# Optimization experiments

Hardware: AMD Instinct MI355X
Metric: run time of the kernel (lower is better)

## Reference

```python
import jax, jax.numpy as jnp
import numpy as np

F = 2048          # frame length = len(window_function) = n_fft
HOP = F // 2      # step_length (overlap=2, perfect reconstruction)
B = 8             # signals / channels
T = 1 << 20       # samples per signal (multiple of HOP)


def setup_inputs() -> dict:
    key = jax.random.key(0)
    x = jax.random.normal(key, (B, T), dtype=jnp.float32)
    # cosine (sine) window, the standard MDCT deringing window
    n = jnp.arange(F, dtype=jnp.float32)
    window = jnp.sin(jnp.pi * (n + 0.5) / F).astype(jnp.float32)
    return {"x": x, "window": window}


def reference(x, window):
    # Batched, fused version of the serial per-frame twiddle-FFT-twiddle MDCT.
    F_ = window.shape[0]
    hop = F_ // 2
    N = F_ // 2                      # output bins per frame (odd-stacked)
    # center=True: pad F/2 zeros on both sides so first/last frames are centered
    xp = jnp.pad(x, ((0, 0), (hop, hop)))
    n_frames = (xp.shape[1] - F_) // hop + 1
    starts = jnp.arange(n_frames) * hop                       # [nf]
    frames = xp[:, starts[:, None] + jnp.arange(F_)]          # [B, nf, F]
    # pre-twiddle: exp(-i*pi*n/(2N)), n = 0..2N-1
    pre = jnp.exp(-1j * jnp.pi * jnp.arange(F_) / F_).astype(jnp.complex64)
    # post-twiddle: exp(-i*pi*n0*(k+0.5)/N), n0 = (N+1)/2
    n0 = (N + 1) / 2.0
    post = jnp.exp(-1j * jnp.pi * n0 * (jnp.arange(N) + 0.5) / N).astype(jnp.complex64)
    # window + pre-twiddle, one batched FFT over all frames, truncate to N bins
    Xc = jnp.fft.fft((frames * window).astype(jnp.complex64) * pre, axis=-1)[..., :N]
    # real part * post-twiddle phase, scale sqrt(1/N)*sqrt(2)
    out = jnp.real(Xc * post) * np.float32(np.sqrt(2.0 / N))
    return out.astype(jnp.float32)          # [B, n_frames, N]
```

## Files before the change

### kernel.cpp

```cpp
#include <hip/hip_runtime.h>
#include <cmath>

#define BATCH   8
#define TLEN    1048576
#define NFRM    1025
#define MROWS   (BATCH * NFRM)

#define SWZ(i) ((i) ^ (((i) >> 4) & 15))

__global__ __launch_bounds__(128)
void mdct_fft_kernel(const float* __restrict__ x,
                     const float* __restrict__ w,
                     float* __restrict__ out)
{
    __shared__ float2 zz[2][512];
    float2* const za = zz[0];
    float2* const zb = zz[1];
    float*  const uf = (float*)zz[1];

    const int r   = blockIdx.x;
    const int tid = threadIdx.x;
    const int b = r / NFRM;
    const int t = r - b * NFRM;

    {
        const float* xb = x + b * TLEN + (t - 1) * 1024;
        {
            const int p  = tid * 4;
            float4 res = {0.0f, 0.0f, 0.0f, 0.0f};
            if (t != NFRM - 1) {
                const int rb = 1532 - p;
                const int fb = 1536 + p;
                float4 xr = *(const float4*)(xb + rb);
                float4 wr = *(const float4*)(w  + rb);
                float4 xf = *(const float4*)(xb + fb);
                float4 wf = *(const float4*)(w  + fb);
                res.x = -(wr.w * xr.w + wf.x * xf.x);
                res.y = -(wr.z * xr.z + wf.y * xf.y);
                res.z = -(wr.y * xr.y + wf.z * xf.z);
                res.w = -(wr.x * xr.x + wf.w * xf.w);
            }
            *(float4*)&uf[p] = res;
        }
        {
            const int p  = 512 + tid * 4;
            float4 res = {0.0f, 0.0f, 0.0f, 0.0f};
            if (t != 0) {
                const int rb = 1532 - p;
                const int fb = p - 512;
                float4 xr = *(const float4*)(xb + rb);
                float4 wr = *(const float4*)(w  + rb);
                float4 xf = *(const float4*)(xb + fb);
                float4 wf = *(const float4*)(w  + fb);
                res.x = wf.x * xf.x - wr.w * xr.w;
                res.y = wf.y * xf.y - wr.z * xr.z;
                res.z = wf.z * xf.z - wr.y * xr.y;
                res.w = wf.w * xf.w - wr.x * xr.x;
            }
            *(float4*)&uf[p] = res;
        }
    }
    __syncthreads();

#pragma unroll
    for (int h = 0; h < 4; ++h) {
        int n = tid + h * 128;
        float re = uf[2 * n];
        float im = uf[1023 - 2 * n];
        float a = (float)(4 * n + 1) * (1.0f / 4096.0f);
        float c = cospif(a), s = sinpif(a);
        za[SWZ(n)] = make_float2(re * c + im * s, im * c - re * s);
    }
    __syncthreads();

    float2* X = za;
    float2* Y = zb;
#pragma unroll
    for (int j = 0; j < 4; ++j) {
        const int ls = 2 * j;
        const int s  = 1 << ls;
        const int mh = 256 >> ls;
        const int p = tid >> ls;
        float2 P0 = X[SWZ(tid)];
        float2 P1 = X[SWZ(tid + 128)];
        float2 P2 = X[SWZ(tid + 256)];
        float2 P3 = X[SWZ(tid + 384)];
        float ang = (float)p * (1.0f / (float)mh);
        float c1 = cospif(ang), s1 = sinpif(ang);
        float c2 = c1 * c1 - s1 * s1, s2 = 2.0f * c1 * s1;
        float c3 = c1 * c2 - s1 * s2, s3 = s1 * c2 + c1 * s2;
        float sax = P0.x + P2.x, say = P0.y + P2.y;
        float sbx = P1.x + P3.x, sby = P1.y + P3.y;
        float dax = P0.x - P2.x, day = P0.y - P2.y;
        float dbx = P1.x - P3.x, dby = P1.y - P3.y;
        const int o = tid + 3 * s * p;
        Y[SWZ(o)] = make_float2(sax + sbx, say + sby);
        float e1x = dax + dby, e1y = day - dbx;
        Y[SWZ(o + s)] = make_float2(e1x * c1 + e1y * s1, e1y * c1 - e1x * s1);
        float e2x = sax - sbx, e2y = say - sby;
        Y[SWZ(o + 2 * s)] = make_float2(e2x * c2 + e2y * s2, e2y * c2 - e2x * s2);
        float e3x = dax - dby, e3y = day + dbx;
        Y[SWZ(o + 3 * s)] = make_float2(e3x * c3 + e3y * s3, e3y * c3 - e3x * s3);
        float2* tmp = X; X = Y; Y = tmp;
        __syncthreads();
    }

#pragma unroll
    for (int hh = 0; hh < 2; ++hh) {
        int k0 = tid + hh * 128;
        float2 A  = X[SWZ(k0)];
        float2 Bv = X[SWZ(k0 + 256)];
        float zr[2] = {A.x + Bv.x, A.x - Bv.x};
        float zi[2] = {A.y + Bv.y, A.y - Bv.y};
#pragma unroll
        for (int h = 0; h < 2; ++h) {
            int k = k0 + h * 256;
            float a = (float)(4 * k + 1) * (1.0f / 4096.0f);
            float c = cospif(a), s = sinpif(a);
            float re = zr[h] * c + zi[h] * s;
            float im = zi[h] * c - zr[h] * s;
            uf[2 * k]        =  re * 0.04419417382415922f;
            uf[1023 - 2 * k] = -im * 0.04419417382415922f;
        }
    }
    __syncthreads();

    *(float4*)&out[r * 1024 + tid * 4]       = *(const float4*)&uf[tid * 4];
    *(float4*)&out[r * 1024 + 512 + tid * 4] = *(const float4*)&uf[512 + tid * 4];
}

extern "C" void kernel_launch(void* const* d_in, const int* in_sizes, int n_in,
                              void* d_out, int out_size, void* d_ws, size_t ws_size,
                              hipStream_t stream) {
    const float* x = (const float*)d_in[0];
    const float* w = (const float*)d_in[1];
    float* out = (float*)d_out;
    (void)d_ws; (void)ws_size;

    mdct_fft_kernel<<<MROWS, 128, 0, stream>>>(x, w, out);
}
```

Before: 93.18 us.

## Assign one frame per wavefront and fuse pre-twiddle into first radix-4 stage

Each 128-thread block now processes two frames, one per 64-lane wavefront, with each wave keeping its own shared-memory buffers. This lets every block-wide __syncthreads be replaced by a wave-level barrier, and the first radix-4 FFT stage is folded into the pre-twiddle pass, saving one shared-memory round trip. Each lane now handles twice as many points, which raises per-thread work and register pressure and doubles LDS use per block.

```diff
diff --git a/kernel.cpp b/kernel.cpp
--- a/kernel.cpp
+++ b/kernel.cpp
@@ -13,20 +13,24 @@
                      const float* __restrict__ w,
                      float* __restrict__ out)
 {
-    __shared__ float2 zz[2][512];
-    float2* const za = zz[0];
-    float2* const zb = zz[1];
-    float*  const uf = (float*)zz[1];
+    __shared__ float2 zz[2][2][512];
+    const int wid  = threadIdx.x >> 6;
+    const int lane = threadIdx.x & 63;
+    float2* const za = zz[wid][0];
+    float2* const zb = zz[wid][1];
+    float*  const uf = (float*)zz[wid][1];
 
-    const int r   = blockIdx.x;
-    const int tid = threadIdx.x;
+    const int r = blockIdx.x * 2 + wid;
     const int b = r / NFRM;
     const int t = r - b * NFRM;
 
-    {
-        const float* xb = x + b * TLEN + (t - 1) * 1024;
+    const float* xb = x + b * TLEN + (t - 1) * 1024;
+
+#pragma unroll
+    for (int sl = 0; sl < 2; ++sl) {
+        const int tt = lane + sl * 64;
         {
-            const int p  = tid * 4;
+            const int p  = tt * 4;
             float4 res = {0.0f, 0.0f, 0.0f, 0.0f};
             if (t != NFRM - 1) {
                 const int rb = 1532 - p;
@@ -43,7 +47,7 @@
             *(float4*)&uf[p] = res;
         }
         {
-            const int p  = 512 + tid * 4;
+            const int p  = 512 + tt * 4;
             float4 res = {0.0f, 0.0f, 0.0f, 0.0f};
             if (t != 0) {
                 const int rb = 1532 - p;
@@ -60,73 +64,119 @@
             *(float4*)&uf[p] = res;
         }
     }
-    __syncthreads();
+    __builtin_amdgcn_wave_barrier();
 
 #pragma unroll
-    for (int h = 0; h < 4; ++h) {
-        int n = tid + h * 128;
-        float re = uf[2 * n];
-        float im = uf[1023 - 2 * n];
-        float a = (float)(4 * n + 1) * (1.0f / 4096.0f);
-        float c = cospif(a), s = sinpif(a);
-        za[SWZ(n)] = make_float2(re * c + im * s, im * c - re * s);
+    for (int sl = 0; sl < 2; ++sl) {
+        const int tt = lane + sl * 64;
+        float px[4], py[4];
+#pragma unroll
+        for (int h = 0; h < 4; ++h) {
+            const int n = tt + h * 128;
+            float re = uf[2 * n];
+            float im = uf[1023 - 2 * n];
+            float a = (float)(4 * n + 1) * (1.0f / 4096.0f);
+            float c = cospif(a), s = sinpif(a);
+            px[h] = re * c + im * s;
+            py[h] = im * c - re * s;
+        }
+        float ang = (float)tt * (1.0f / 256.0f);
+        float c1 = cospif(ang), s1 = sinpif(ang);
+        float c2 = c1 * c1 - s1 * s1, s2 = 2.0f * c1 * s1;
+        float c3 = c1 * c2 - s1 * s2, s3 = s1 * c2 + c1 * s2;
+        float sax = px[0] + px[2], say = py[0] + py[2];
+        float sbx = px[1] + px[3], sby = py[1] + py[3];
+        float dax = px[0] - px[2], day = py[0] - py[2];
+        float dbx = px[1] - px[3], dby = py[1] - py[3];
+        const int o = 4 * tt;
+        za[SWZ(o)] = make_float2(sax + sbx, say + sby);
+        float e1x = dax + dby, e1y = day - dbx;
+        za[SWZ(o + 1)] = make_float2(e1x * c1 + e1y * s1, e1y * c1 - e1x * s1);
+        float e2x = sax - sbx, e2y = say - sby;
+        za[SWZ(o + 2)] = make_float2(e2x * c2 + e2y * s2, e2y * c2 - e2x * s2);
+        float e3x = dax - dby, e3y = day + dbx;
+        za[SWZ(o + 3)] = make_float2(e3x * c3 + e3y * s3, e3y * c3 - e3x * s3);
     }
-    __syncthreads();
+    __builtin_amdgcn_wave_barrier();
 
     float2* X = za;
     float2* Y = zb;
 #pragma unroll
-    for (int j = 0; j < 4; ++j) {
+    for (int j = 1; j < 4; ++j) {
         const int ls = 2 * j;
         const int s  = 1 << ls;
         const int mh = 256 >> ls;
-        const int p = tid >> ls;
-        float2 P0 = X[SWZ(tid)];
-        float2 P1 = X[SWZ(tid + 128)];
-        float2 P2 = X[SWZ(tid + 256)];
-        float2 P3 = X[SWZ(tid + 384)];
-        float ang = (float)p * (1.0f / (float)mh);
-        float c1 = cospif(ang), s1 = sinpif(ang);
-        float c2 = c1 * c1 - s1 * s1, s2 = 2.0f * c1 * s1;
-        float c3 = c1 * c2 - s1 * s2, s3 = s1 * c2 + c1 * s2;
-        float sax = P0.x + P2.x, say = P0.y + P2.y;
-        float sbx = P1.x + P3.x, sby = P1.y + P3.y;
-        float dax = P0.x - P2.x, day = P0.y - P2.y;
-        float dbx = P1.x - P3.x, dby = P1.y - P3.y;
-        const int o = tid + 3 * s * p;
-        Y[SWZ(o)] = make_float2(sax + sbx, say + sby);
-        float e1x = dax + dby, e1y = day - dbx;
-        Y[SWZ(o + s)] = make_float2(e1x * c1 + e1y * s1, e1y * c1 - e1x * s1);
-        float e2x = sax - sbx, e2y = say - sby;
-        Y[SWZ(o + 2 * s)] = make_float2(e2x * c2 + e2y * s2, e2y * c2 - e2x * s2);
-        float e3x = dax - dby, e3y = day + dbx;
-        Y[SWZ(o + 3 * s)] = make_float2(e3x * c3 + e3y * s3, e3y * c3 - e3x * s3);
+#pragma unroll
+        for (int sl = 0; sl < 2; ++sl) {
+            const int tt = lane + sl * 64;
+            const int p  = tt >> ls;
+            float2 P0 = X[SWZ(tt)];
+            float2 P1 = X[SWZ(tt + 128)];
+            float2 P2 = X[SWZ(tt + 256)];
+            float2 P3 = X[SWZ(tt + 384)];
+            float ang = (float)p * (1.0f / (float)mh);
+            float c1 = cospif(ang), s1 = sinpif(ang);
+            float c2 = c1 * c1 - s1 * s1, s2 = 2.0f * c1 * s1;
+            float c3 = c1 * c2 - s1 * s2, s3 = s1 * c2 + c1 * s2;
+            float sax = P0.x + P2.x, say = P0.y + P2.y;
+            float sbx = P1.x + P3.x, sby = P1.y + P3.y;
+            float dax = P0.x - P2.x, day = P0.y - P2.y;
+            float dbx = P1.x - P3.x, dby = P1.y - P3.y;
+            const int o = tt + 3 * s * p;
+            Y[SWZ(o)] = make_float2(sax + sbx, say + sby);
+            float e1x = dax + dby, e1y = day - dbx;
+            Y[SWZ(o + s)] = make_float2(e1x * c1 + e1y * s1, e1y * c1 - e1x * s1);
+            float e2x = sax - sbx, e2y = say - sby;
+            Y[SWZ(o + 2 * s)] = make_float2(e2x * c2 + e2y * s2, e2y * c2 - e2x * s2);
+            float e3x = dax - dby, e3y = day + dbx;
+            Y[SWZ(o + 3 * s)] = make_float2(e3x * c3 + e3y * s3, e3y * c3 - e3x * s3);
+        }
         float2* tmp = X; X = Y; Y = tmp;
-        __syncthreads();
+        __builtin_amdgcn_wave_barrier();
     }
 
+    float2 Av[4], Bv[4];
 #pragma unroll
-    for (int hh = 0; hh < 2; ++hh) {
-        int k0 = tid + hh * 128;
-        float2 A  = X[SWZ(k0)];
-        float2 Bv = X[SWZ(k0 + 256)];
-        float zr[2] = {A.x + Bv.x, A.x - Bv.x};
-        float zi[2] = {A.y + Bv.y, A.y - Bv.y};
+    for (int sl = 0; sl < 2; ++sl) {
+        const int tt = lane + sl * 64;
 #pragma unroll
-        for (int h = 0; h < 2; ++h) {
-            int k = k0 + h * 256;
-            float a = (float)(4 * k + 1) * (1.0f / 4096.0f);
-            float c = cospif(a), s = sinpif(a);
-            float re = zr[h] * c + zi[h] * s;
-            float im = zi[h] * c - zr[h] * s;
-            uf[2 * k]        =  re * 0.04419417382415922f;
-            uf[1023 - 2 * k] = -im * 0.04419417382415922f;
+        for (int hh = 0; hh < 2; ++hh) {
+            const int k0 = tt + hh * 128;
+            Av[sl * 2 + hh] = X[SWZ(k0)];
+            Bv[sl * 2 + hh] = X[SWZ(k0 + 256)];
         }
     }
-    __syncthreads();
+    __builtin_amdgcn_wave_barrier();
+#pragma unroll
+    for (int sl = 0; sl < 2; ++sl) {
+        const int tt = lane + sl * 64;
+#pragma unroll
+        for (int hh = 0; hh < 2; ++hh) {
+            const int k0 = tt + hh * 128;
+            const float2 A  = Av[sl * 2 + hh];
+            const float2 Bq = Bv[sl * 2 + hh];
+            float zr[2] = {A.x + Bq.x, A.x - Bq.x};
+            float zi[2] = {A.y + Bq.y, A.y - Bq.y};
+#pragma unroll
+            for (int h = 0; h < 2; ++h) {
+                const int k = k0 + h * 256;
+                float a = (float)(4 * k + 1) * (1.0f / 4096.0f);
+                float c = cospif(a), s = sinpif(a);
+                float re = zr[h] * c + zi[h] * s;
+                float im = zi[h] * c - zr[h] * s;
+                uf[2 * k]        =  re * 0.04419417382415922f;
+                uf[1023 - 2 * k] = -im * 0.04419417382415922f;
+            }
+        }
+    }
+    __builtin_amdgcn_wave_barrier();
 
-    *(float4*)&out[r * 1024 + tid * 4]       = *(const float4*)&uf[tid * 4];
-    *(float4*)&out[r * 1024 + 512 + tid * 4] = *(const float4*)&uf[512 + tid * 4];
+#pragma unroll
+    for (int sl = 0; sl < 2; ++sl) {
+        const int tt = lane + sl * 64;
+        *(float4*)&out[r * 1024 + tt * 4]       = *(const float4*)&uf[tt * 4];
+        *(float4*)&out[r * 1024 + 512 + tt * 4] = *(const float4*)&uf[512 + tt * 4];
+    }
 }
 
 extern "C" void kernel_launch(void* const* d_in, const int* in_sizes, int n_in,
@@ -137,5 +187,6 @@
     float* out = (float*)d_out;
     (void)d_ws; (void)ws_size;
 
-    mdct_fft_kernel<<<MROWS, 128, 0, stream>>>(x, w, out);
+    static_assert(MROWS % 2 == 0, "two frames per block");
+    mdct_fft_kernel<<<MROWS / 2, 128, 0, stream>>>(x, w, out);
 }
```

Result: slower. 95.59 us (+2.6%).
